# Kernel optimization log

Hardware: AMD Instinct MI355X
Metric: run time of the kernel (lower is better)

## Reference

```python
import jax, jax.numpy as jnp
import numpy as np

N_NODES = 50000
N_EDGES = 800000
NFEAT, NHID, NCLASS = 512, 128, 40


def spmm(row, col, w, x, n):
    # sparse adj (COO) @ dense x : gather source rows, scale, segment-sum into dest
    return jax.ops.segment_sum(w[:, None] * x[col], row, num_segments=n)


def setup_inputs() -> dict:
    key = jax.random.key(0)
    ks = jax.random.split(key, 8)
    x = jax.random.normal(ks[0], (N_NODES, NFEAT), dtype=jnp.float32)
    edge_row = jax.random.randint(ks[1], (N_EDGES,), 0, N_NODES, dtype=jnp.int32)
    edge_col = jax.random.randint(ks[2], (N_EDGES,), 0, N_NODES, dtype=jnp.int32)
    edge_weight = jax.random.uniform(ks[3], (N_EDGES,), dtype=jnp.float32)
    # Glorot-style init as in GraphConvolution.reset_parameters
    w1 = jax.random.normal(ks[4], (NFEAT, NHID), dtype=jnp.float32) / np.sqrt(NFEAT)
    b1 = jax.random.normal(ks[5], (NHID,), dtype=jnp.float32) * 0.01
    w2 = jax.random.normal(ks[6], (NHID, NCLASS), dtype=jnp.float32) / np.sqrt(NHID)
    b2 = jax.random.normal(ks[7], (NCLASS,), dtype=jnp.float32) * 0.01
    return {"x": x, "edge_row": edge_row, "edge_col": edge_col,
            "edge_weight": edge_weight, "w1": w1, "b1": b1, "w2": w2, "b2": b2}


def reference(x, edge_row, edge_col, edge_weight, w1, b1, w2, b2):
    n = x.shape[0]
    # layer 1: relu(adj @ (x @ w1) + b1)   (dropout is identity in eval mode)
    h = jax.nn.relu(spmm(edge_row, edge_col, edge_weight, x @ w1, n) + b1)
    # layer 2: adj @ (h @ w2) + b2
    out = spmm(edge_row, edge_col, edge_weight, h @ w2, n) + b2
    return out
```

## Files before the change

kernel.cpp:

```cpp
#include <hip/hip_runtime.h>
#include <hip/hip_bf16.h>
#include <cstddef>


typedef float f32x4 __attribute__((ext_vector_type(4)));
typedef short bf16x8 __attribute__((ext_vector_type(8)));

static __device__ __forceinline__ short f2bf(float f) {
    __hip_bfloat16 b = __float2bfloat16(f);
    return *reinterpret_cast<short*>(&b);
}
static __device__ __forceinline__ float bflo(unsigned u) {
    union { unsigned i; float f; } v; v.i = u << 16; return v.f;
}
static __device__ __forceinline__ float bfhi(unsigned u) {
    union { unsigned i; float f; } v; v.i = u & 0xFFFF0000u; return v.f;
}
static __device__ __forceinline__ unsigned pack2bf(float lo, float hi) {
    unsigned a = (unsigned short)f2bf(lo);
    unsigned b = (unsigned short)f2bf(hi);
    return a | (b << 16);
}

typedef const __attribute__((address_space(1))) void* gas_ptr;
typedef __attribute__((address_space(3))) void* las_ptr;
static __device__ __forceinline__ void gload16(const void* g, void* l) {
    __builtin_amdgcn_global_load_lds((gas_ptr)g, (las_ptr)l, 16, 0, 0);
}

__global__ __launch_bounds__(256) void prep_kernel(
    const float* __restrict__ W1, short* __restrict__ W1Tb,
    const float* __restrict__ W2, short* __restrict__ W2Ts,
    int* __restrict__ cur, int N)
{
    int idx = blockIdx.x * 256 + threadIdx.x;
    if (idx < 65536) {
        int k = idx >> 7, n = idx & 127;
        W1Tb[n * 512 + k] = f2bf(W1[idx]);
    } else if (idx < 65536 + 6144) {
        int i2 = idx - 65536;
        int n = i2 >> 7, k = i2 & 127;
        W2Ts[i2 ^ ((n & 7) << 3)] = (n < 40) ? f2bf(W2[k * 40 + n]) : (short)0;
    } else if (idx < 65536 + 6144 + N) {
        cur[idx - 65536 - 6144] = 0;
    }
}

__global__ __launch_bounds__(256, 6) void gemm1_mfma_kernel(
    const float* __restrict__ X, const short* __restrict__ W1Tb,
    short* __restrict__ XW1b, int M)
{
    __shared__ __align__(16) short As[64 * 40];
    __shared__ __align__(16) short Bs[128 * 40];

    const int tid = threadIdx.x;
    const int w   = tid >> 6;
    const int l   = tid & 63;
    const int l15 = l & 15;
    const int l4  = l >> 4;
    const int row0 = blockIdx.x * 64;
    const int rb   = (w & 1) * 32;
    const int cb   = (w >> 1) * 64;

    const int sr = tid >> 2;
    const int sc = (tid & 3) * 8;
    const int ga = row0 + sr < M ? row0 + sr : M - 1;
    const float* ax = X + (size_t)ga * 512 + sc;
    const int bn = tid >> 1;
    const int bk = (tid & 1) * 16;
    const short* bw = W1Tb + (size_t)bn * 512 + bk;

    f32x4 acc[2][4];
#pragma unroll
    for (int i = 0; i < 2; ++i)
#pragma unroll
        for (int f = 0; f < 4; ++f) acc[i][f] = (f32x4)0.f;

    float4 a0 = *(const float4*)(ax);
    float4 a1 = *(const float4*)(ax + 4);
    bf16x8 bv0 = *(const bf16x8*)(bw);
    bf16x8 bv1 = *(const bf16x8*)(bw + 8);

#pragma unroll
    for (int kt = 0; kt < 16; ++kt) {
        __syncthreads();
        bf16x8 av;
        av[0]=f2bf(a0.x); av[1]=f2bf(a0.y); av[2]=f2bf(a0.z); av[3]=f2bf(a0.w);
        av[4]=f2bf(a1.x); av[5]=f2bf(a1.y); av[6]=f2bf(a1.z); av[7]=f2bf(a1.w);
        *(bf16x8*)&As[sr * 40 + sc] = av;
        *(bf16x8*)&Bs[bn * 40 + bk] = bv0;
        *(bf16x8*)&Bs[bn * 40 + bk + 8] = bv1;
        __syncthreads();

        if (kt < 15) {
            a0 = *(const float4*)(ax + (kt + 1) * 32);
            a1 = *(const float4*)(ax + (kt + 1) * 32 + 4);
            bv0 = *(const bf16x8*)(bw + (kt + 1) * 32);
            bv1 = *(const bf16x8*)(bw + (kt + 1) * 32 + 8);
        }

        bf16x8 af0 = *(const bf16x8*)&As[(rb + l15) * 40 + l4 * 8];
        bf16x8 af1 = *(const bf16x8*)&As[(rb + 16 + l15) * 40 + l4 * 8];
#pragma unroll
        for (int f = 0; f < 4; ++f) {
            const bf16x8 bf_ = *(const bf16x8*)&Bs[(cb + f * 16 + l15) * 40 + l4 * 8];
            acc[0][f] = __builtin_amdgcn_mfma_f32_16x16x32_bf16(af0, bf_, acc[0][f], 0, 0, 0);
            acc[1][f] = __builtin_amdgcn_mfma_f32_16x16x32_bf16(af1, bf_, acc[1][f], 0, 0, 0);
        }
    }

#pragma unroll
    for (int i = 0; i < 2; ++i)
#pragma unroll
        for (int r = 0; r < 4; ++r) {
            const int row = row0 + rb + i * 16 + l4 * 4 + r;
            if (row < M) {
#pragma unroll
                for (int f = 0; f < 4; ++f)
                    XW1b[(size_t)row * 128 + cb + f * 16 + l15] = f2bf(acc[i][f][r]);
            }
        }
}

__global__ __launch_bounds__(256) void hist_kernel(const int* __restrict__ row,
                                                   int* __restrict__ counts, int E)
{
    int e = blockIdx.x * 256 + threadIdx.x;
    if (e < E) atomicAdd(&counts[row[e]], 1);
}

__global__ __launch_bounds__(256) void scan1_kernel(const int* __restrict__ counts,
                                                    int* __restrict__ excl,
                                                    int* __restrict__ bsum, int N)
{
    __shared__ int s[256];
    const int t = threadIdx.x;
    const int i = blockIdx.x * 256 + t;
    int v = (i < N) ? counts[i] : 0;
    s[t] = v; __syncthreads();
#pragma unroll
    for (int off = 1; off < 256; off <<= 1) {
        int tmp = (t >= off) ? s[t - off] : 0;
        __syncthreads();
        s[t] += tmp;
        __syncthreads();
    }
    if (i < N) excl[i] = s[t] - v;
    if (t == 255) bsum[blockIdx.x] = s[255];
}

__global__ __launch_bounds__(256) void scan2_kernel(int* __restrict__ bsum, int NB)
{
    __shared__ int s[256];
    const int t = threadIdx.x;
    int v = (t < NB) ? bsum[t] : 0;
    s[t] = v; __syncthreads();
#pragma unroll
    for (int off = 1; off < 256; off <<= 1) {
        int tmp = (t >= off) ? s[t - off] : 0;
        __syncthreads();
        s[t] += tmp;
        __syncthreads();
    }
    if (t < NB) bsum[t] = s[t] - v;
}

__global__ __launch_bounds__(256) void scan3_kernel(int* __restrict__ rowptr,
                                                    const int* __restrict__ bsum,
                                                    int* __restrict__ cur, int N, int E)
{
    int i = blockIdx.x * 256 + threadIdx.x;
    if (i < N) {
        int v = rowptr[i] + bsum[blockIdx.x];
        rowptr[i] = v;
        cur[i] = v;
    }
    if (i == 0) rowptr[N] = E;
}

__global__ __launch_bounds__(256) void sortedges_kernel(
    const int* __restrict__ row, const int* __restrict__ col,
    const float* __restrict__ w, int* __restrict__ cur,
    int2* __restrict__ se, int E)
{
    int e = blockIdx.x * 256 + threadIdx.x;
    if (e < E) {
        int r = row[e];
        int pos = atomicAdd(&cur[r], 1);
        se[pos] = make_int2(col[e], __float_as_int(w[e]));
    }
}

__global__ __launch_bounds__(256) void segment1_kernel(
    const int* __restrict__ rowptr, const int2* __restrict__ se,
    const uint4* __restrict__ x4, const float* __restrict__ b1,
    uint4* __restrict__ hb4, int N)
{
    const int w    = threadIdx.x >> 6;
    const int lane = threadIdx.x & 63;
    const int qt   = lane >> 4;
    const int ql   = lane & 15;
    const int r = blockIdx.x * 4 + w;
    if (r >= N) return;

    float acc[8];
    if (qt == 0) {
        const float4 ba = *(const float4*)(b1 + 8 * ql);
        const float4 bb = *(const float4*)(b1 + 8 * ql + 4);
        acc[0]=ba.x; acc[1]=ba.y; acc[2]=ba.z; acc[3]=ba.w;
        acc[4]=bb.x; acc[5]=bb.y; acc[6]=bb.z; acc[7]=bb.w;
    } else {
#pragma unroll
        for (int i = 0; i < 8; ++i) acc[i] = 0.f;
    }

    int j = rowptr[r];
    const int end = rowptr[r + 1];
    for (; j + 7 < end; j += 8) {
        const int2 ea = se[j + qt];
        const int2 eb = se[j + 4 + qt];
        const uint4 ua = x4[(size_t)ea.x * 16 + ql];
        const uint4 ub = x4[(size_t)eb.x * 16 + ql];
        const float wa = __int_as_float(ea.y), wb = __int_as_float(eb.y);
        acc[0] = fmaf(wa, bflo(ua.x), acc[0]); acc[1] = fmaf(wa, bfhi(ua.x), acc[1]);
        acc[2] = fmaf(wa, bflo(ua.y), acc[2]); acc[3] = fmaf(wa, bfhi(ua.y), acc[3]);
        acc[4] = fmaf(wa, bflo(ua.z), acc[4]); acc[5] = fmaf(wa, bfhi(ua.z), acc[5]);
        acc[6] = fmaf(wa, bflo(ua.w), acc[6]); acc[7] = fmaf(wa, bfhi(ua.w), acc[7]);
        acc[0] = fmaf(wb, bflo(ub.x), acc[0]); acc[1] = fmaf(wb, bfhi(ub.x), acc[1]);
        acc[2] = fmaf(wb, bflo(ub.y), acc[2]); acc[3] = fmaf(wb, bfhi(ub.y), acc[3]);
        acc[4] = fmaf(wb, bflo(ub.z), acc[4]); acc[5] = fmaf(wb, bfhi(ub.z), acc[5]);
        acc[6] = fmaf(wb, bflo(ub.w), acc[6]); acc[7] = fmaf(wb, bfhi(ub.w), acc[7]);
    }
    for (; j < end; j += 4) {
        const int idx = j + qt;
        const int ic  = idx < end ? idx : end - 1;
        const int2 e  = se[ic];
        const float wt = idx < end ? __int_as_float(e.y) : 0.f;
        const uint4 u = x4[(size_t)e.x * 16 + ql];
        acc[0] = fmaf(wt, bflo(u.x), acc[0]); acc[1] = fmaf(wt, bfhi(u.x), acc[1]);
        acc[2] = fmaf(wt, bflo(u.y), acc[2]); acc[3] = fmaf(wt, bfhi(u.y), acc[3]);
        acc[4] = fmaf(wt, bflo(u.z), acc[4]); acc[5] = fmaf(wt, bfhi(u.z), acc[5]);
        acc[6] = fmaf(wt, bflo(u.w), acc[6]); acc[7] = fmaf(wt, bfhi(u.w), acc[7]);
    }
#pragma unroll
    for (int i = 0; i < 8; ++i) {
        acc[i] += __shfl_xor(acc[i], 16);
        acc[i] += __shfl_xor(acc[i], 32);
    }
    if (qt == 0) {
        uint4 o;
        o.x = pack2bf(fmaxf(acc[0], 0.f), fmaxf(acc[1], 0.f));
        o.y = pack2bf(fmaxf(acc[2], 0.f), fmaxf(acc[3], 0.f));
        o.z = pack2bf(fmaxf(acc[4], 0.f), fmaxf(acc[5], 0.f));
        o.w = pack2bf(fmaxf(acc[6], 0.f), fmaxf(acc[7], 0.f));
        hb4[(size_t)r * 16 + ql] = o;
    }
}

__global__ __launch_bounds__(256) void gemm2_mfma_kernel(
    const short* __restrict__ hb, const short* __restrict__ W2Ts,
    unsigned short* __restrict__ Y48, int M)
{
    __shared__ __align__(16) short Ws[48 * 128];

    const int tid = threadIdx.x;
    const int w   = tid >> 6;
    const int l   = tid & 63;
    const int l15 = l & 15;
    const int l4  = l >> 4;
    const int row0 = blockIdx.x * 64 + w * 16;

    {
        const char* src = (const char*)W2Ts;
        char* dst = (char*)Ws;
#pragma unroll
        for (int i = 0; i < 3; ++i)
            gload16(src + i * 4096 + tid * 16, dst + i * 4096 + tid * 16);
    }
    __syncthreads();

    f32x4 acc[3];
#pragma unroll
    for (int f = 0; f < 3; ++f) acc[f] = (f32x4)0.f;

    const int rr = row0 + l15;
    const int cr = rr < M ? rr : M - 1;
    const short* hp = hb + (size_t)cr * 128 + l4 * 8;
    const int swz = (l15 & 7) << 3;

#pragma unroll
    for (int kt = 0; kt < 4; ++kt) {
        const bf16x8 a = *(const bf16x8*)(hp + kt * 32);
#pragma unroll
        for (int f = 0; f < 3; ++f) {
            const int si = ((f * 16 + l15) * 128 + kt * 32 + l4 * 8) ^ swz;
            const bf16x8 b = *(const bf16x8*)&Ws[si];
            acc[f] = __builtin_amdgcn_mfma_f32_16x16x32_bf16(a, b, acc[f], 0, 0, 0);
        }
    }

#pragma unroll
    for (int r = 0; r < 4; ++r) {
        const int row = row0 + l4 * 4 + r;
        if (row < M) {
#pragma unroll
            for (int f = 0; f < 3; ++f)
                Y48[(size_t)row * 48 + f * 16 + l15] = (unsigned short)f2bf(acc[f][r]);
        }
    }
}

__global__ __launch_bounds__(256) void segment2_kernel(
    const int* __restrict__ rowptr, const int2* __restrict__ se,
    const uint2* __restrict__ h48, const float* __restrict__ b2,
    float* __restrict__ out, int N)
{
    const int w    = threadIdx.x >> 6;
    const int lane = threadIdx.x & 63;
    const int qt   = lane >> 4;
    const int ql   = lane & 15;
    const int r = blockIdx.x * 4 + w;
    if (r >= N) return;

    float acc[4];
    if (qt == 0 && ql < 10) {
        const float4 bb = *(const float4*)(b2 + 4 * ql);
        acc[0]=bb.x; acc[1]=bb.y; acc[2]=bb.z; acc[3]=bb.w;
    } else {
#pragma unroll
        for (int i = 0; i < 4; ++i) acc[i] = 0.f;
    }

    int j = rowptr[r];
    const int end = rowptr[r + 1];
    for (; j + 7 < end; j += 8) {
        const int2 ea = se[j + qt];
        const int2 eb = se[j + 4 + qt];
        const uint2 ua = h48[(size_t)ea.x * 12 + ql];
        const uint2 ub = h48[(size_t)eb.x * 12 + ql];
        const float wa = __int_as_float(ea.y), wb = __int_as_float(eb.y);
        acc[0] = fmaf(wa, bflo(ua.x), acc[0]); acc[1] = fmaf(wa, bfhi(ua.x), acc[1]);
        acc[2] = fmaf(wa, bflo(ua.y), acc[2]); acc[3] = fmaf(wa, bfhi(ua.y), acc[3]);
        acc[0] = fmaf(wb, bflo(ub.x), acc[0]); acc[1] = fmaf(wb, bfhi(ub.x), acc[1]);
        acc[2] = fmaf(wb, bflo(ub.y), acc[2]); acc[3] = fmaf(wb, bfhi(ub.y), acc[3]);
    }
    for (; j < end; j += 4) {
        const int idx = j + qt;
        const int ic  = idx < end ? idx : end - 1;
        const int2 e  = se[ic];
        const float wt = idx < end ? __int_as_float(e.y) : 0.f;
        const uint2 u = h48[(size_t)e.x * 12 + ql];
        acc[0] = fmaf(wt, bflo(u.x), acc[0]); acc[1] = fmaf(wt, bfhi(u.x), acc[1]);
        acc[2] = fmaf(wt, bflo(u.y), acc[2]); acc[3] = fmaf(wt, bfhi(u.y), acc[3]);
    }
#pragma unroll
    for (int i = 0; i < 4; ++i) {
        acc[i] += __shfl_xor(acc[i], 16);
        acc[i] += __shfl_xor(acc[i], 32);
    }
    if (qt == 0 && ql < 10) {
        float4 o; o.x = acc[0]; o.y = acc[1]; o.z = acc[2]; o.w = acc[3];
        *(float4*)(out + (size_t)r * 40 + 4 * ql) = o;
    }
}

extern "C" void kernel_launch(void* const* d_in, const int* in_sizes, int n_in,
                              void* d_out, int out_size, void* d_ws, size_t ws_size,
                              hipStream_t stream)
{
    const float* x  = (const float*)d_in[0];
    const int* erow = (const int*)d_in[1];
    const int* ecol = (const int*)d_in[2];
    const float* ew = (const float*)d_in[3];
    const float* w1 = (const float*)d_in[4];
    const float* b1 = (const float*)d_in[5];
    const float* w2 = (const float*)d_in[6];
    const float* b2 = (const float*)d_in[7];
    float* out = (float*)d_out;

    const int N = in_sizes[0] / 512;
    const int E = in_sizes[1];
    const int NB = (N + 255) / 256;

    short* w1tb = (short*)d_ws;
    short* w2ts = w1tb + 65536;
    short* xw1b = w2ts + 8192;
    short* hb   = xw1b + (size_t)N * 128;
    int* rowptr = (int*)(hb + (size_t)N * 128);
    int* cur    = rowptr + (N + 1);
    int* bsum   = cur + N;
    int2* se    = (int2*)(bsum + 256 + ((N + 1) & 1));
    short* h48  = xw1b;

    prep_kernel<<<(65536 + 6144 + N + 255) / 256, 256, 0, stream>>>(w1, w1tb, w2, w2ts, cur, N);
    hist_kernel<<<(E + 255) / 256, 256, 0, stream>>>(erow, cur, E);
    scan1_kernel<<<NB, 256, 0, stream>>>(cur, rowptr, bsum, N);
    scan2_kernel<<<1, 256, 0, stream>>>(bsum, NB);
    scan3_kernel<<<NB, 256, 0, stream>>>(rowptr, bsum, cur, N, E);
    sortedges_kernel<<<(E + 255) / 256, 256, 0, stream>>>(erow, ecol, ew, cur, se, E);

    gemm1_mfma_kernel<<<(N + 63) / 64, 256, 0, stream>>>(x, w1tb, xw1b, N);
    segment1_kernel<<<(N + 3) / 4, 256, 0, stream>>>(rowptr, se,
                                                     (const uint4*)xw1b, b1,
                                                     (uint4*)hb, N);

    gemm2_mfma_kernel<<<(N + 63) / 64, 256, 0, stream>>>(hb, w2ts,
                                                         (unsigned short*)h48, N);
    segment2_kernel<<<(N + 3) / 4, 256, 0, stream>>>(rowptr, se,
                                                     (const uint2*)h48, b2, out, N);
}
```

Measured before the change: 189.2 us.

## Fuse scan stages, co-launch edge sort with GEMM1, fuse segment1 with GEMM2

Merges the scan2 and scan3 kernels so that every block redoes the small block-sum scan itself. The edge-sort work now runs as extra blocks of the GEMM1 launch, so the two independent jobs share one launch and can overlap. Segment1 is fused with GEMM2: each 4-row block stages its relu'd hidden rows in shared memory and one wave runs the MFMA against W2 held in LDS, which removes the hb round trip and two launches. The cost is that every aggregation block now loads W2 into LDS, and the MFMA runs on a 16-row tile of which only 4 rows are valid, wasting most of its work.

```diff
diff --git a/kernel.cpp b/kernel.cpp
--- a/kernel.cpp
+++ b/kernel.cpp
@@ -46,14 +46,81 @@
     }
 }
 
-__global__ __launch_bounds__(256, 6) void gemm1_mfma_kernel(
+__global__ __launch_bounds__(256) void hist_kernel(const int* __restrict__ row,
+                                                   int* __restrict__ counts, int E)
+{
+    int e = blockIdx.x * 256 + threadIdx.x;
+    if (e < E) atomicAdd(&counts[row[e]], 1);
+}
+
+__global__ __launch_bounds__(256) void scan1_kernel(const int* __restrict__ counts,
+                                                    int* __restrict__ excl,
+                                                    int* __restrict__ bsum, int N)
+{
+    __shared__ int s[256];
+    const int t = threadIdx.x;
+    const int i = blockIdx.x * 256 + t;
+    int v = (i < N) ? counts[i] : 0;
+    s[t] = v; __syncthreads();
+#pragma unroll
+    for (int off = 1; off < 256; off <<= 1) {
+        int tmp = (t >= off) ? s[t - off] : 0;
+        __syncthreads();
+        s[t] += tmp;
+        __syncthreads();
+    }
+    if (i < N) excl[i] = s[t] - v;
+    if (t == 255) bsum[blockIdx.x] = s[255];
+}
+
+__global__ __launch_bounds__(256) void scan23_kernel(int* __restrict__ rowptr,
+                                                     const int* __restrict__ bsum,
+                                                     int* __restrict__ cur,
+                                                     int N, int E, int NB)
+{
+    __shared__ int s[256];
+    const int t = threadIdx.x;
+    int v = (t < NB) ? bsum[t] : 0;
+    s[t] = v; __syncthreads();
+#pragma unroll
+    for (int off = 1; off < 256; off <<= 1) {
+        int tmp = (t >= off) ? s[t - off] : 0;
+        __syncthreads();
+        s[t] += tmp;
+        __syncthreads();
+    }
+    const int add = (blockIdx.x > 0) ? s[blockIdx.x - 1] : 0;
+    const int i = blockIdx.x * 256 + t;
+    if (i < N) {
+        int v2 = rowptr[i] + add;
+        rowptr[i] = v2;
+        cur[i] = v2;
+    }
+    if (i == 0) rowptr[N] = E;
+}
+
+__global__ __launch_bounds__(256, 6) void gemm1_sort_kernel(
     const float* __restrict__ X, const short* __restrict__ W1Tb,
-    short* __restrict__ XW1b, int M)
+    short* __restrict__ XW1b, int M, int G1,
+    const int* __restrict__ erow, const int* __restrict__ ecol,
+    const float* __restrict__ ew, int* __restrict__ cur,
+    int2* __restrict__ se, int E)
 {
     __shared__ __align__(16) short As[64 * 40];
     __shared__ __align__(16) short Bs[128 * 40];
 
     const int tid = threadIdx.x;
+
+    if (blockIdx.x >= G1) {
+        int e = (blockIdx.x - G1) * 256 + tid;
+        if (e < E) {
+            int r = erow[e];
+            int pos = atomicAdd(&cur[r], 1);
+            se[pos] = make_int2(ecol[e], __float_as_int(ew[e]));
+        }
+        return;
+    }
+
     const int w   = tid >> 6;
     const int l   = tid & 63;
     const int l15 = l & 15;
@@ -122,86 +189,30 @@
         }
 }
 
-__global__ __launch_bounds__(256) void hist_kernel(const int* __restrict__ row,
-                                                   int* __restrict__ counts, int E)
-{
-    int e = blockIdx.x * 256 + threadIdx.x;
-    if (e < E) atomicAdd(&counts[row[e]], 1);
-}
-
-__global__ __launch_bounds__(256) void scan1_kernel(const int* __restrict__ counts,
-                                                    int* __restrict__ excl,
-                                                    int* __restrict__ bsum, int N)
-{
-    __shared__ int s[256];
-    const int t = threadIdx.x;
-    const int i = blockIdx.x * 256 + t;
-    int v = (i < N) ? counts[i] : 0;
-    s[t] = v; __syncthreads();
-#pragma unroll
-    for (int off = 1; off < 256; off <<= 1) {
-        int tmp = (t >= off) ? s[t - off] : 0;
-        __syncthreads();
-        s[t] += tmp;
-        __syncthreads();
-    }
-    if (i < N) excl[i] = s[t] - v;
-    if (t == 255) bsum[blockIdx.x] = s[255];
-}
-
-__global__ __launch_bounds__(256) void scan2_kernel(int* __restrict__ bsum, int NB)
-{
-    __shared__ int s[256];
-    const int t = threadIdx.x;
-    int v = (t < NB) ? bsum[t] : 0;
-    s[t] = v; __syncthreads();
-#pragma unroll
-    for (int off = 1; off < 256; off <<= 1) {
-        int tmp = (t >= off) ? s[t - off] : 0;
-        __syncthreads();
-        s[t] += tmp;
-        __syncthreads();
-    }
-    if (t < NB) bsum[t] = s[t] - v;
-}
-
-__global__ __launch_bounds__(256) void scan3_kernel(int* __restrict__ rowptr,
-                                                    const int* __restrict__ bsum,
-                                                    int* __restrict__ cur, int N, int E)
-{
-    int i = blockIdx.x * 256 + threadIdx.x;
-    if (i < N) {
-        int v = rowptr[i] + bsum[blockIdx.x];
-        rowptr[i] = v;
-        cur[i] = v;
-    }
-    if (i == 0) rowptr[N] = E;
-}
-
-__global__ __launch_bounds__(256) void sortedges_kernel(
-    const int* __restrict__ row, const int* __restrict__ col,
-    const float* __restrict__ w, int* __restrict__ cur,
-    int2* __restrict__ se, int E)
-{
-    int e = blockIdx.x * 256 + threadIdx.x;
-    if (e < E) {
-        int r = row[e];
-        int pos = atomicAdd(&cur[r], 1);
-        se[pos] = make_int2(col[e], __float_as_int(w[e]));
-    }
-}
-
-__global__ __launch_bounds__(256) void segment1_kernel(
+__global__ __launch_bounds__(256) void seg1g2_kernel(
     const int* __restrict__ rowptr, const int2* __restrict__ se,
     const uint4* __restrict__ x4, const float* __restrict__ b1,
-    uint4* __restrict__ hb4, int N)
-{
-    const int w    = threadIdx.x >> 6;
-    const int lane = threadIdx.x & 63;
+    const short* __restrict__ W2Ts, unsigned short* __restrict__ h48, int N)
+{
+    __shared__ __align__(16) short Ws[48 * 128];
+    __shared__ __align__(16) short Hs[16 * 136];
+
+    const int tid  = threadIdx.x;
+    const int w    = tid >> 6;
+    const int lane = tid & 63;
     const int qt   = lane >> 4;
     const int ql   = lane & 15;
-    const int r = blockIdx.x * 4 + w;
-    if (r >= N) return;
+    const int row0q = blockIdx.x * 4;
+    const int r  = row0q + w;
+    const int rc = r < N ? r : N - 1;
+
+    {
+        const char* src = (const char*)W2Ts;
+        char* dst = (char*)Ws;
+#pragma unroll
+        for (int i = 0; i < 3; ++i)
+            gload16(src + i * 4096 + tid * 16, dst + i * 4096 + tid * 16);
+    }
 
     float acc[8];
     if (qt == 0) {
@@ -214,8 +225,8 @@
         for (int i = 0; i < 8; ++i) acc[i] = 0.f;
     }
 
-    int j = rowptr[r];
-    const int end = rowptr[r + 1];
+    int j = rowptr[rc];
+    const int end = rowptr[rc + 1];
     for (; j + 7 < end; j += 8) {
         const int2 ea = se[j + qt];
         const int2 eb = se[j + 4 + qt];
@@ -253,59 +264,38 @@
         o.y = pack2bf(fmaxf(acc[2], 0.f), fmaxf(acc[3], 0.f));
         o.z = pack2bf(fmaxf(acc[4], 0.f), fmaxf(acc[5], 0.f));
         o.w = pack2bf(fmaxf(acc[6], 0.f), fmaxf(acc[7], 0.f));
-        hb4[(size_t)r * 16 + ql] = o;
-    }
-}
-
-__global__ __launch_bounds__(256) void gemm2_mfma_kernel(
-    const short* __restrict__ hb, const short* __restrict__ W2Ts,
-    unsigned short* __restrict__ Y48, int M)
-{
-    __shared__ __align__(16) short Ws[48 * 128];
-
-    const int tid = threadIdx.x;
-    const int w   = tid >> 6;
-    const int l   = tid & 63;
-    const int l15 = l & 15;
-    const int l4  = l >> 4;
-    const int row0 = blockIdx.x * 64 + w * 16;
-
-    {
-        const char* src = (const char*)W2Ts;
-        char* dst = (char*)Ws;
-#pragma unroll
-        for (int i = 0; i < 3; ++i)
-            gload16(src + i * 4096 + tid * 16, dst + i * 4096 + tid * 16);
+        *(uint4*)&Hs[w * 136 + ql * 8] = o;
     }
     __syncthreads();
 
-    f32x4 acc[3];
-#pragma unroll
-    for (int f = 0; f < 3; ++f) acc[f] = (f32x4)0.f;
-
-    const int rr = row0 + l15;
-    const int cr = rr < M ? rr : M - 1;
-    const short* hp = hb + (size_t)cr * 128 + l4 * 8;
-    const int swz = (l15 & 7) << 3;
-
-#pragma unroll
-    for (int kt = 0; kt < 4; ++kt) {
-        const bf16x8 a = *(const bf16x8*)(hp + kt * 32);
-#pragma unroll
-        for (int f = 0; f < 3; ++f) {
-            const int si = ((f * 16 + l15) * 128 + kt * 32 + l4 * 8) ^ swz;
-            const bf16x8 b = *(const bf16x8*)&Ws[si];
-            acc[f] = __builtin_amdgcn_mfma_f32_16x16x32_bf16(a, b, acc[f], 0, 0, 0);
-        }
-    }
-
-#pragma unroll
-    for (int r = 0; r < 4; ++r) {
-        const int row = row0 + l4 * 4 + r;
-        if (row < M) {
-#pragma unroll
-            for (int f = 0; f < 3; ++f)
-                Y48[(size_t)row * 48 + f * 16 + l15] = (unsigned short)f2bf(acc[f][r]);
+    if (tid < 64) {
+        const int l15 = lane & 15;
+        const int l4  = lane >> 4;
+        const int swz = (l15 & 7) << 3;
+        f32x4 acc2[3];
+#pragma unroll
+        for (int f = 0; f < 3; ++f) acc2[f] = (f32x4)0.f;
+#pragma unroll
+        for (int kt = 0; kt < 4; ++kt) {
+            const bf16x8 a = *(const bf16x8*)&Hs[l15 * 136 + kt * 32 + l4 * 8];
+#pragma unroll
+            for (int f = 0; f < 3; ++f) {
+                const int si = ((f * 16 + l15) * 128 + kt * 32 + l4 * 8) ^ swz;
+                const bf16x8 b = *(const bf16x8*)&Ws[si];
+                acc2[f] = __builtin_amdgcn_mfma_f32_16x16x32_bf16(a, b, acc2[f], 0, 0, 0);
+            }
+        }
+        if (l4 == 0) {
+#pragma unroll
+            for (int rr = 0; rr < 4; ++rr) {
+                const int grow = row0q + rr;
+                if (grow < N) {
+#pragma unroll
+                    for (int f = 0; f < 3; ++f)
+                        h48[(size_t)grow * 48 + f * 16 + l15] =
+                            (unsigned short)f2bf(acc2[f][rr]);
+                }
+            }
         }
     }
 }
@@ -385,27 +375,26 @@
     short* w1tb = (short*)d_ws;
     short* w2ts = w1tb + 65536;
     short* xw1b = w2ts + 8192;
-    short* hb   = xw1b + (size_t)N * 128;
-    int* rowptr = (int*)(hb + (size_t)N * 128);
+    short* h48  = xw1b + (size_t)N * 128;
+    int* rowptr = (int*)(h48 + (size_t)N * 128);
     int* cur    = rowptr + (N + 1);
     int* bsum   = cur + N;
     int2* se    = (int2*)(bsum + 256 + ((N + 1) & 1));
-    short* h48  = xw1b;
 
     prep_kernel<<<(65536 + 6144 + N + 255) / 256, 256, 0, stream>>>(w1, w1tb, w2, w2ts, cur, N);
     hist_kernel<<<(E + 255) / 256, 256, 0, stream>>>(erow, cur, E);
     scan1_kernel<<<NB, 256, 0, stream>>>(cur, rowptr, bsum, N);
-    scan2_kernel<<<1, 256, 0, stream>>>(bsum, NB);
-    scan3_kernel<<<NB, 256, 0, stream>>>(rowptr, bsum, cur, N, E);
-    sortedges_kernel<<<(E + 255) / 256, 256, 0, stream>>>(erow, ecol, ew, cur, se, E);
-
-    gemm1_mfma_kernel<<<(N + 63) / 64, 256, 0, stream>>>(x, w1tb, xw1b, N);
-    segment1_kernel<<<(N + 3) / 4, 256, 0, stream>>>(rowptr, se,
-                                                     (const uint4*)xw1b, b1,
-                                                     (uint4*)hb, N);
-
-    gemm2_mfma_kernel<<<(N + 63) / 64, 256, 0, stream>>>(hb, w2ts,
-                                                         (unsigned short*)h48, N);
+    scan23_kernel<<<NB, 256, 0, stream>>>(rowptr, bsum, cur, N, E, NB);
+
+    const int G1 = (N + 63) / 64;
+    const int GS = (E + 255) / 256;
+    gemm1_sort_kernel<<<G1 + GS, 256, 0, stream>>>(x, w1tb, xw1b, N, G1,
+                                                   erow, ecol, ew, cur, se, E);
+
+    seg1g2_kernel<<<(N + 3) / 4, 256, 0, stream>>>(rowptr, se,
+                                                   (const uint4*)xw1b, b1,
+                                                   w2ts, (unsigned short*)h48, N);
+
     segment2_kernel<<<(N + 3) / 4, 256, 0, stream>>>(rowptr, se,
                                                      (const uint2*)h48, b2, out, N);
 }
```

Result: faster. 155.4 us, median of 2 (-17.9%).
